# Kernel optimization log

Hardware: AMD Instinct MI355X
Metric: run time of the kernel (lower is better)

The kernel has to match this reference:

```python
import jax, jax.numpy as jnp
import numpy as np

C = 64
D = C // 8  # Q/K channel dim
B, H, W = 4, 64, 64


def setup_inputs() -> dict:
    key = jax.random.key(0)
    ks = jax.random.split(key, 4)
    x = jax.random.normal(ks[0], (B, C, H, W), dtype=jnp.float32)
    # 1x1 conv weights collapse to matrices [out_ch, in_ch]
    Wq = jax.random.normal(ks[1], (D, C), dtype=jnp.float32) * (1.0 / np.sqrt(C))
    Wk = jax.random.normal(ks[2], (D, C), dtype=jnp.float32) * (1.0 / np.sqrt(C))
    Wv = jax.random.normal(ks[3], (C, C), dtype=jnp.float32) * (1.0 / np.sqrt(C))
    bq = jnp.zeros((D,), jnp.float32)
    bk = jnp.zeros((D,), jnp.float32)
    bv = jnp.zeros((C,), jnp.float32)
    gamma = jnp.zeros((1,), jnp.float32)  # initialized to zero as in the module
    return {"x": x, "Wq": Wq, "bq": bq, "Wk": Wk, "bk": bk,
            "Wv": Wv, "bv": bv, "gamma": gamma}


def reference(x, Wq, bq, Wk, bk, Wv, bv, gamma):
    b, c, h, w = x.shape
    n = h * w
    xf = x.reshape(b, c, n)  # [B, C, N]
    # 1x1 convs == per-pixel linear projections
    q = jnp.einsum('dc,bcn->bdn', Wq, xf) + bq[None, :, None]  # [B, D, N]
    k = jnp.einsum('dc,bcn->bdn', Wk, xf) + bk[None, :, None]  # [B, D, N]
    v = jnp.einsum('ec,bcn->ben', Wv, xf) + bv[None, :, None]  # [B, C, N]
    # energy[b, i, j] = sum_d q[b, d, i] * k[b, d, j]  (query index i, key index j)
    energy = jnp.einsum('bdi,bdj->bij', q, k)  # [B, N, N]
    attn = jax.nn.softmax(energy, axis=-1)     # [B, N, N]
    # out[b, c, i] = sum_j v[b, c, j] * attn[b, i, j]
    out = jnp.einsum('bcj,bij->bci', v, attn)  # [B, C, N]
    out = out.reshape(b, c, h, w)
    return gamma[0] * out + x
```

## Files before the change

kernel.cpp:

```cpp
#include <hip/hip_runtime.h>
#include <hip/hip_bf16.h>

#define NPIX 4096

typedef __attribute__((ext_vector_type(16))) float f32x16;
typedef __attribute__((ext_vector_type(8))) short short8;

__device__ inline short f2bf(float f) {
  unsigned u = __float_as_uint(f);
  u += 0x7FFF + ((u >> 16) & 1);
  return (short)(u >> 16);
}

__device__ inline void gload16(const short* g, short* l) {
  __builtin_amdgcn_global_load_lds(
      (const __attribute__((address_space(1))) void*)g,
      (__attribute__((address_space(3))) void*)l, 16, 0, 0);
}

__global__ __launch_bounds__(256) void proj_kernel(
    const float* __restrict__ x,
    const float* __restrict__ Wq, const float* __restrict__ bq,
    const float* __restrict__ Wk, const float* __restrict__ bk,
    const float* __restrict__ Wv, const float* __restrict__ bv,
    short* __restrict__ Qp, short* __restrict__ Kp, short* __restrict__ Vi)
{
  const int job = blockIdx.x >> 6;
  const int p = (blockIdx.x & 63) * 256 + threadIdx.x;
  const int b = p >> 12, n = p & 4095;
  const float* xb = x + ((size_t)b << 18) + n;

  float xv[64];
#pragma unroll
  for (int c = 0; c < 64; ++c) xv[c] = xb[(size_t)c << 12];

  if (job < 2) {
    const float* W    = job ? Wk : Wq;
    const float* bias = job ? bk : bq;
    float a[8];
#pragma unroll
    for (int d = 0; d < 8; ++d) {
      float acc = bias[d];
#pragma unroll
      for (int c = 0; c < 64; ++c) acc = fmaf(W[d * 64 + c], xv[c], acc);
      a[d] = acc;
    }
    short8 o;
    if (job == 0) {
#pragma unroll
      for (int d = 0; d < 8; ++d) o[d] = f2bf(a[d] * 1.44269504f);
      *(short8*)(Qp + (size_t)p * 8) = o;
    } else {
#pragma unroll
      for (int d = 0; d < 8; ++d) o[d] = f2bf(a[d]);
      *(short8*)(Kp + (size_t)p * 8) = o;
    }
  } else {
    const int e0 = (job - 2) * 8;
    const size_t base = ((size_t)(b * 512 + (n >> 3)) * 64) * 8 + (n & 7);
#pragma unroll
    for (int i = 0; i < 8; ++i) {
      float acc = bv[e0 + i];
#pragma unroll
      for (int c = 0; c < 64; ++c) acc = fmaf(Wv[(e0 + i) * 64 + c], xv[c], acc);
      Vi[base + (size_t)(e0 + i) * 8] = f2bf(acc);
    }
  }
}

__device__ inline void pk_swap(const float* p, short8& A0, short8& A1) {
  unsigned u[8];
#pragma unroll
  for (int j = 0; j < 8; ++j)
    asm("v_cvt_pk_bf16_f32 %0, %1, %2" : "=v"(u[j]) : "v"(p[2 * j]), "v"(p[2 * j + 1]));
  asm("v_permlane32_swap_b32 %0, %1" : "+v"(u[0]), "+v"(u[2]));
  asm("v_permlane32_swap_b32 %0, %1" : "+v"(u[1]), "+v"(u[3]));
  asm("v_permlane32_swap_b32 %0, %1" : "+v"(u[4]), "+v"(u[6]));
  asm("v_permlane32_swap_b32 %0, %1" : "+v"(u[5]), "+v"(u[7]));
  union { unsigned w[4]; short8 s; } c0, c1;
  c0.w[0] = u[0]; c0.w[1] = u[1]; c0.w[2] = u[2]; c0.w[3] = u[3];
  c1.w[0] = u[4]; c1.w[1] = u[5]; c1.w[2] = u[6]; c1.w[3] = u[7];
  A0 = c0.s; A1 = c1.s;
}

__global__ __launch_bounds__(512, 2) void attn_kernel(
    const short* __restrict__ Qp, const short* __restrict__ Kp,
    const short* __restrict__ Vi,
    short* __restrict__ accB, float* __restrict__ psumW)
{
  __shared__ short kLds[2][1024];
  __shared__ short vLds[2][8192];

  const int tid  = threadIdx.x;
  const int wv   = tid >> 6;
  const int lane = tid & 63;
  const int lo   = lane & 31;
  const int hi   = lane >> 5;

  const int bid = blockIdx.x;
  const int ks  = bid & 7;
  const int qg  = (bid >> 3) & 15;
  const int b   = bid >> 7;
  const int Qgbase = (b << 12) + qg * 256 + wv * 32;
  const int slot = ks;

  short8 qf = {};
  if (hi == 0) qf = *(const short8*)(Qp + (size_t)(Qgbase + lo) * 8);

  const short* ksrc = Kp + ((size_t)(b << 12) + ks * 512) * 8;
  const short* vsrc = Vi + (size_t)b * 262144 + (size_t)ks * 32768;

  auto stage = [&](int c, int buf) {
    const short* vs = vsrc + (size_t)c * 8192;
    gload16(vs + (size_t)tid * 8,         &vLds[buf][(tid & ~63) * 8]);
    gload16(vs + (size_t)(tid + 512) * 8, &vLds[buf][((tid + 512) & ~63) * 8]);
    if (tid < 128)
      gload16(ksrc + (size_t)c * 1024 + (size_t)tid * 8, &kLds[buf][(tid & ~63) * 8]);
  };

  f32x16 acc0 = {}, acc1 = {};
  float psum = 0.f;
  const f32x16 z = {};

  stage(0, 0);
  __syncthreads();

  for (int c = 0; c < 4; ++c) {
    if (c < 3) stage(c + 1, (c + 1) & 1);
    const int buf = c & 1;
#pragma unroll
    for (int i = 0; i < 4; ++i) {
      short8 kf = *(const short8*)&kLds[buf][(i * 32 + lo) * 8];
      f32x16 en = __builtin_amdgcn_mfma_f32_32x32x16_bf16(kf, qf, z, 0, 0, 0);
      float p[16];
#pragma unroll
      for (int j = 0; j < 16; ++j) p[j] = __builtin_amdgcn_exp2f(en[j]);
#pragma unroll
      for (int j = 0; j < 16; ++j) psum += p[j];
      short8 a0, a1;
      pk_swap(p, a0, a1);
      short8 v00 = *(const short8*)&vLds[buf][(i * 4 + hi) * 512 + lo * 8];
      short8 v01 = *(const short8*)&vLds[buf][(i * 4 + hi) * 512 + (32 + lo) * 8];
      short8 v10 = *(const short8*)&vLds[buf][(i * 4 + 2 + hi) * 512 + lo * 8];
      short8 v11 = *(const short8*)&vLds[buf][(i * 4 + 2 + hi) * 512 + (32 + lo) * 8];
      __builtin_amdgcn_s_setprio(1);
      acc0 = __builtin_amdgcn_mfma_f32_32x32x16_bf16(a0, v00, acc0, 0, 0, 0);
      acc1 = __builtin_amdgcn_mfma_f32_32x32x16_bf16(a0, v01, acc1, 0, 0, 0);
      acc0 = __builtin_amdgcn_mfma_f32_32x32x16_bf16(a1, v10, acc0, 0, 0, 0);
      acc1 = __builtin_amdgcn_mfma_f32_32x32x16_bf16(a1, v11, acc1, 0, 0, 0);
      __builtin_amdgcn_s_setprio(0);
    }
    __syncthreads();
  }

  float pfull = psum + __shfl_xor(psum, 32);
  if (hi == 0) psumW[slot * 16384 + Qgbase + lo] = pfull;

#pragma unroll
  for (int r = 0; r < 16; ++r) {
    const int q = (r & 3) + 8 * (r >> 2) + 4 * hi;
    const size_t base = ((size_t)(slot * 16384 + Qgbase + q)) << 6;
    accB[base + lo]      = f2bf(acc0[r]);
    accB[base + 32 + lo] = f2bf(acc1[r]);
  }
}

__global__ __launch_bounds__(256) void reduce_kernel(
    const short* __restrict__ accB, const float* __restrict__ psumW,
    const float* __restrict__ x, const float* __restrict__ gamma,
    float* __restrict__ out)
{
  __shared__ float accLds[64][65];
  __shared__ float sInv[64];

  const int tid = threadIdx.x;
  const int Qg0 = blockIdx.x * 64;
  const float g = gamma[0];

  if (tid < 64) {
    float s = 0.f;
#pragma unroll
    for (int sl = 0; sl < 8; ++sl) s += psumW[sl * 16384 + Qg0 + tid];
    sInv[tid] = g / s;
  }

  const int e2 = tid & 31;
  const int qr = tid >> 5;
#pragma unroll
  for (int qsw = 0; qsw < 8; ++qsw) {
    const int qq = qr + qsw * 8;
    float s0 = 0.f, s1 = 0.f;
#pragma unroll
    for (int sl = 0; sl < 8; ++sl) {
      const unsigned u = *(const unsigned*)&accB[(((size_t)(sl * 16384 + Qg0 + qq)) << 6) + e2 * 2];
      s0 += __uint_as_float(u << 16);
      s1 += __uint_as_float(u & 0xFFFF0000u);
    }
    accLds[qq][e2 * 2]     = s0;
    accLds[qq][e2 * 2 + 1] = s1;
  }
  __syncthreads();

  const int q  = tid & 63;
  const int er = tid >> 6;
  const int b  = (Qg0 + q) >> 12;
  const int n  = (Qg0 + q) & 4095;
  const float si = sInv[q];
#pragma unroll
  for (int k = 0; k < 16; ++k) {
    const int e = er + k * 4;
    const size_t idx = ((size_t)(b * 64 + e) << 12) + n;
    out[idx] = fmaf(si, accLds[q][e], x[idx]);
  }
}

extern "C" void kernel_launch(void* const* d_in, const int* in_sizes, int n_in,
                              void* d_out, int out_size, void* d_ws, size_t ws_size,
                              hipStream_t stream) {
  const float* x     = (const float*)d_in[0];
  const float* Wq    = (const float*)d_in[1];
  const float* bq    = (const float*)d_in[2];
  const float* Wk    = (const float*)d_in[3];
  const float* bk    = (const float*)d_in[4];
  const float* Wv    = (const float*)d_in[5];
  const float* bv    = (const float*)d_in[6];
  const float* gamma = (const float*)d_in[7];
  float* out = (float*)d_out;

  short* ws    = (short*)d_ws;
  short* Qp    = ws;
  short* Kp    = ws + 131072;
  short* Vi    = ws + 262144;
  short* accB  = ws + 1310720;
  float* psumW = (float*)(ws + 9699328);

  proj_kernel<<<640, 256, 0, stream>>>(x, Wq, bq, Wk, bk, Wv, bv, Qp, Kp, Vi);
  attn_kernel<<<512, 512, 0, stream>>>(Qp, Kp, Vi, accB, psumW);
  reduce_kernel<<<256, 256, 0, stream>>>(accB, psumW, x, gamma, out);
}
```

Before: 107.8 us.

## Fuse split-K reduction into attention kernel via last-block atomic counter

Removes the separate reduce kernel. Each attention block bumps a per-(batch, query-group) counter after writing its partial results. The eighth block to finish then performs the cross-slot reduction, normalization and residual add, reusing shared memory. This saves one kernel launch and its dependency gap, but serializes the reduction onto the last-arriving blocks, which adds tail latency. It also adds fences and atomics, and the counters are reset inside the projection kernel.

```diff
diff --git a/kernel.cpp b/kernel.cpp
--- a/kernel.cpp
+++ b/kernel.cpp
@@ -23,8 +23,11 @@
     const float* __restrict__ Wq, const float* __restrict__ bq,
     const float* __restrict__ Wk, const float* __restrict__ bk,
     const float* __restrict__ Wv, const float* __restrict__ bv,
-    short* __restrict__ Qp, short* __restrict__ Kp, short* __restrict__ Vi)
+    short* __restrict__ Qp, short* __restrict__ Kp, short* __restrict__ Vi,
+    int* __restrict__ counters)
 {
+  if (blockIdx.x == 0 && threadIdx.x < 64) counters[threadIdx.x] = 0;
+
   const int job = blockIdx.x >> 6;
   const int p = (blockIdx.x & 63) * 256 + threadIdx.x;
   const int b = p >> 12, n = p & 4095;
@@ -86,10 +89,17 @@
 __global__ __launch_bounds__(512, 2) void attn_kernel(
     const short* __restrict__ Qp, const short* __restrict__ Kp,
     const short* __restrict__ Vi,
-    short* __restrict__ accB, float* __restrict__ psumW)
+    short* __restrict__ accB, float* __restrict__ psumW,
+    int* __restrict__ counters,
+    const float* __restrict__ x, const float* __restrict__ gamma,
+    float* __restrict__ out)
 {
-  __shared__ short kLds[2][1024];
-  __shared__ short vLds[2][8192];
+  __shared__ __align__(16) char smem[36872];
+  short (*kLds)[1024] = (short (*)[1024])smem;
+  short (*vLds)[8192] = (short (*)[8192])(smem + 4096);
+  float (*accLds)[65] = (float (*)[65])smem;
+  float* sInvL        = (float*)(smem + 33280);
+  int*   lastF        = (int*)(smem + 34304);
 
   const int tid  = threadIdx.x;
   const int wv   = tid >> 6;
@@ -155,7 +165,6 @@
 
   float pfull = psum + __shfl_xor(psum, 32);
   if (hi == 0) psumW[slot * 16384 + Qgbase + lo] = pfull;
-
 #pragma unroll
   for (int r = 0; r < 16; ++r) {
     const int q = (r & 3) + 8 * (r >> 2) + 4 * hi;
@@ -163,54 +172,63 @@
     accB[base + lo]      = f2bf(acc0[r]);
     accB[base + 32 + lo] = f2bf(acc1[r]);
   }
-}
-
-__global__ __launch_bounds__(256) void reduce_kernel(
-    const short* __restrict__ accB, const float* __restrict__ psumW,
-    const float* __restrict__ x, const float* __restrict__ gamma,
-    float* __restrict__ out)
-{
-  __shared__ float accLds[64][65];
-  __shared__ float sInv[64];
-
-  const int tid = threadIdx.x;
-  const int Qg0 = blockIdx.x * 64;
+
+  __threadfence();
+  __syncthreads();
+  if (tid == 0) {
+    const int old = atomicAdd(&counters[b * 16 + qg], 1);
+    *lastF = (old == 7);
+  }
+  __syncthreads();
+  const bool last = (*lastF != 0);
+  __syncthreads();
+  if (!last) return;
+  __threadfence();
+
+  const int Qbase = (b << 12) + qg * 256;
   const float g = gamma[0];
-
-  if (tid < 64) {
+  if (tid < 256) {
     float s = 0.f;
 #pragma unroll
-    for (int sl = 0; sl < 8; ++sl) s += psumW[sl * 16384 + Qg0 + tid];
-    sInv[tid] = g / s;
-  }
-
-  const int e2 = tid & 31;
-  const int qr = tid >> 5;
-#pragma unroll
-  for (int qsw = 0; qsw < 8; ++qsw) {
-    const int qq = qr + qsw * 8;
-    float s0 = 0.f, s1 = 0.f;
-#pragma unroll
-    for (int sl = 0; sl < 8; ++sl) {
-      const unsigned u = *(const unsigned*)&accB[(((size_t)(sl * 16384 + Qg0 + qq)) << 6) + e2 * 2];
-      s0 += __uint_as_float(u << 16);
-      s1 += __uint_as_float(u & 0xFFFF0000u);
-    }
-    accLds[qq][e2 * 2]     = s0;
-    accLds[qq][e2 * 2 + 1] = s1;
-  }
-  __syncthreads();
-
-  const int q  = tid & 63;
-  const int er = tid >> 6;
-  const int b  = (Qg0 + q) >> 12;
-  const int n  = (Qg0 + q) & 4095;
-  const float si = sInv[q];
-#pragma unroll
-  for (int k = 0; k < 16; ++k) {
-    const int e = er + k * 4;
-    const size_t idx = ((size_t)(b * 64 + e) << 12) + n;
-    out[idx] = fmaf(si, accLds[q][e], x[idx]);
+    for (int sl = 0; sl < 8; ++sl) s += psumW[sl * 16384 + Qbase + tid];
+    sInvL[tid] = g / s;
+  }
+
+#pragma unroll
+  for (int pass = 0; pass < 2; ++pass) {
+    const int q128 = pass * 128;
+    __syncthreads();
+    {
+      const int e2 = tid & 31;
+      const int qr = tid >> 5;
+#pragma unroll
+      for (int sw = 0; sw < 8; ++sw) {
+        const int qq = qr + sw * 16;
+        const int gq = Qbase + q128 + qq;
+        float s0 = 0.f, s1 = 0.f;
+#pragma unroll
+        for (int sl = 0; sl < 8; ++sl) {
+          const unsigned u = *(const unsigned*)&accB[(((size_t)(sl * 16384 + gq)) << 6) + e2 * 2];
+          s0 += __uint_as_float(u << 16);
+          s1 += __uint_as_float(u & 0xFFFF0000u);
+        }
+        accLds[qq][e2 * 2]     = s0;
+        accLds[qq][e2 * 2 + 1] = s1;
+      }
+    }
+    __syncthreads();
+    {
+      const int q  = tid & 127;
+      const int er = tid >> 7;
+      const int n  = qg * 256 + q128 + q;
+      const float si = sInvL[q128 + q];
+#pragma unroll
+      for (int k = 0; k < 16; ++k) {
+        const int e = er + k * 4;
+        const size_t idx = ((size_t)(b * 64 + e) << 12) + n;
+        out[idx] = fmaf(si, accLds[q][e], x[idx]);
+      }
+    }
   }
 }
 
@@ -227,14 +245,14 @@
   const float* gamma = (const float*)d_in[7];
   float* out = (float*)d_out;
 
-  short* ws    = (short*)d_ws;
-  short* Qp    = ws;
-  short* Kp    = ws + 131072;
-  short* Vi    = ws + 262144;
-  short* accB  = ws + 1310720;
-  float* psumW = (float*)(ws + 9699328);
-
-  proj_kernel<<<640, 256, 0, stream>>>(x, Wq, bq, Wk, bk, Wv, bv, Qp, Kp, Vi);
-  attn_kernel<<<512, 512, 0, stream>>>(Qp, Kp, Vi, accB, psumW);
-  reduce_kernel<<<256, 256, 0, stream>>>(accB, psumW, x, gamma, out);
-}
+  short* ws     = (short*)d_ws;
+  short* Qp     = ws;
+  short* Kp     = ws + 131072;
+  short* Vi     = ws + 262144;
+  short* accB   = ws + 1310720;
+  float* psumW  = (float*)(ws + 9699328);
+  int* counters = (int*)(ws + 9961472);
+
+  proj_kernel<<<640, 256, 0, stream>>>(x, Wq, bq, Wk, bk, Wv, bv, Qp, Kp, Vi, counters);
+  attn_kernel<<<512, 512, 0, stream>>>(Qp, Kp, Vi, accB, psumW, counters, x, gamma, out);
+}
```

Measured after the change: 245.8 us. +128.0%, slower.
